# Performance work log

Hardware: AMD Instinct MI355X
Metric: run time of the kernel (lower is better)

Reference implementation:

```python
import jax, jax.numpy as jnp
import numpy as np

NUM_EXPERTS = 8
TOP_K = 2
HIDDEN = 2048
INTER = 2048
SWIGLU_LIMIT = 7.0
BATCH, SEQ = 4, 2048


def setup_inputs() -> dict:
    key = jax.random.key(0)
    k0, k1, k2, k3, k4 = jax.random.split(key, 5)
    x = jax.random.normal(k0, (BATCH, SEQ, HIDDEN), jnp.float32)
    Wr = jax.random.normal(k1, (HIDDEN, NUM_EXPERTS), jnp.float32) * 0.02
    Wg = jax.random.normal(k2, (NUM_EXPERTS, HIDDEN, INTER), jnp.float32) * 0.02
    Wu = jax.random.normal(k3, (NUM_EXPERTS, HIDDEN, INTER), jnp.float32) * 0.02
    Wd = jax.random.normal(k4, (NUM_EXPERTS, INTER, HIDDEN), jnp.float32) * 0.02
    return {"hidden_states": x, "Wr": Wr, "Wg": Wg, "Wu": Wu, "Wd": Wd}


def reference(hidden_states, Wr, Wg, Wu, Wd):
    # Router: logits [B,S,E], top-k over experts, softmax over the k logits.
    router_logits = jnp.einsum('bsh,he->bse', hidden_states, Wr)
    topk_logits, selected = jax.lax.top_k(router_logits, TOP_K)  # [B,S,K]
    router_probs = jax.nn.softmax(topk_logits, axis=-1)          # [B,S,K]

    # Per-expert masked-dense SwiGLU. Because the Dense layers have no bias,
    # Expert(x * mask) == Expert(x) at selected positions and the combine
    # weight is 0 elsewhere, so running on unmasked x is mathematically
    # identical to the original's masked-input formulation.
    out = jnp.zeros_like(hidden_states)
    for e in range(NUM_EXPERTS):  # fixed structural loop over experts
        w_e = jnp.where(selected == e, router_probs, 0.0).sum(axis=-1, keepdims=True)  # [B,S,1]
        g = jnp.einsum('bsh,hi->bsi', hidden_states, Wg[e])
        g = jnp.clip(jax.nn.silu(g), -SWIGLU_LIMIT, SWIGLU_LIMIT)
        u = jnp.einsum('bsh,hi->bsi', hidden_states, Wu[e])
        h = jnp.einsum('bsi,ih->bsh', g * u, Wd[e])
        out = out + h * w_e
    return out
```

## Files before the change

### kernel.cpp

```cpp
#include <hip/hip_runtime.h>

#define TOKENS 8192
#define HID 2048
#define NEXP 8
#define NT 32
#define MAXTILES 72

typedef float f32x4 __attribute__((ext_vector_type(4)));
typedef short bf16x8 __attribute__((ext_vector_type(8)));

#define WS_XBF     0ULL
#define WS_ACT     33554432ULL
#define WS_WCAT    100663296ULL
#define WS_WDT     234881024ULL
#define WS_ROWTOK  301989888ULL
#define WS_ROWPROB 302055424ULL
#define WS_EIDX    302120960ULL
#define WS_PROBS   302186496ULL
#define WS_META    302252032ULL
#define WS_SLOT    302253056ULL

__device__ __forceinline__ unsigned short f2bf(float f) {
    union { float f; unsigned int u; } a; a.f = f;
    unsigned int r = a.u + 0x7fffu + ((a.u >> 16) & 1u);
    return (unsigned short)(r >> 16);
}

__device__ __forceinline__ float bf2f(unsigned int lo16) {
    union { unsigned int u; float f; } x; x.u = lo16 << 16; return x.f;
}

__device__ __forceinline__ void gload16(void* ldsdst, const void* gsrc) {
    __builtin_amdgcn_global_load_lds(
        (const __attribute__((address_space(1))) void*)gsrc,
        (__attribute__((address_space(3))) void*)ldsdst, 16, 0, 0);
}

#define BAR asm volatile("s_barrier" ::: "memory")
#define VM4 asm volatile("s_waitcnt vmcnt(4)" ::: "memory")
#define VM0 asm volatile("s_waitcnt vmcnt(0)" ::: "memory")

__global__ __launch_bounds__(256) void router_kernel(
    const float* __restrict__ x, const float* __restrict__ Wr,
    unsigned short* __restrict__ xbf, int2* __restrict__ eidx,
    float2* __restrict__ probs, int* __restrict__ meta) {
    __shared__ float wrt[NEXP * HID];
    int tid = threadIdx.x;
    for (int f = tid; f < HID * NEXP; f += 256) {
        int i = f >> 3, e = f & 7;
        wrt[e * HID + i] = Wr[f];
    }
    __syncthreads();
    int w = tid >> 6, l = tid & 63;
#pragma unroll 1
    for (int ti = 0; ti < 4; ++ti) {
        int tok = blockIdx.x * 16 + w * 4 + ti;
        const float4* xr = (const float4*)(x + (size_t)tok * HID);
        float acc[NEXP];
#pragma unroll
        for (int e = 0; e < NEXP; ++e) acc[e] = 0.f;
        unsigned long long* xbr = (unsigned long long*)(xbf + (size_t)tok * HID);
#pragma unroll
        for (int it = 0; it < 8; ++it) {
            float4 v = xr[it * 64 + l];
            int k0 = (it * 64 + l) * 4;
#pragma unroll
            for (int e = 0; e < NEXP; ++e) {
                float4 wv = *(const float4*)&wrt[e * HID + k0];
                acc[e] += v.x * wv.x + v.y * wv.y + v.z * wv.z + v.w * wv.w;
            }
            unsigned long long pk = (unsigned long long)f2bf(v.x)
                                  | ((unsigned long long)f2bf(v.y) << 16)
                                  | ((unsigned long long)f2bf(v.z) << 32)
                                  | ((unsigned long long)f2bf(v.w) << 48);
            int qi = ((k0 >> 5) << 3) + (((k0 >> 2) & 3) << 1) + ((k0 >> 4) & 1);
            xbr[qi] = pk;
        }
#pragma unroll
        for (int e = 0; e < NEXP; ++e) {
#pragma unroll
            for (int d = 1; d < 64; d <<= 1) acc[e] += __shfl_xor(acc[e], d, 64);
        }
        if (l == 0) {
            int e0 = 0; float v0 = acc[0];
#pragma unroll
            for (int e = 1; e < NEXP; ++e) if (acc[e] > v0) { v0 = acc[e]; e0 = e; }
            int e1 = -1; float v1 = 0.f;
#pragma unroll
            for (int e = 0; e < NEXP; ++e)
                if (e != e0 && (e1 < 0 || acc[e] > v1)) { v1 = acc[e]; e1 = e; }
            float a = __expf(v1 - v0);
            float inv = 1.f / (1.f + a);
            int2 ei; ei.x = e0; ei.y = e1;
            float2 pp; pp.x = inv; pp.y = a * inv;
            eidx[tok] = ei;
            probs[tok] = pp;
            atomicAdd(&meta[e0], 1);
            atomicAdd(&meta[e1], 1);
        }
    }
}

__global__ __launch_bounds__(256) void convert_kernel(
    const float* __restrict__ Wg, const float* __restrict__ Wu,
    const float* __restrict__ Wd, unsigned short* __restrict__ wcat,
    unsigned short* __restrict__ wdt) {
    int mz = blockIdx.z;
    int mat = mz >> 3, e = mz & 7;
    const float* W = (mat == 0 ? Wg : (mat == 1 ? Wu : Wd)) + (size_t)e * HID * HID;
    int kb = blockIdx.y * 64, nb = blockIdx.x * 64;
    __shared__ unsigned short t[64][68];
    int tid = threadIdx.x;
    int kr = tid >> 4;
    int nc = (tid & 15) * 4;
#pragma unroll
    for (int ki = 0; ki < 4; ++ki) {
        int k = kr + ki * 16;
        float4 v = *(const float4*)&W[(size_t)(kb + k) * HID + nb + nc];
        t[nc + 0][k] = f2bf(v.x);
        t[nc + 1][k] = f2bf(v.y);
        t[nc + 2][k] = f2bf(v.z);
        t[nc + 3][k] = f2bf(v.w);
    }
    __syncthreads();
    int n = tid >> 2;
    int seg = tid & 3;
    int gn = nb + n;
    unsigned short* orow;
    if (mat < 2)
        orow = wcat + ((size_t)e * 4096 + (gn >> 4) * 32 + mat * 16 + (gn & 15)) * HID;
    else
        orow = wdt + ((size_t)e * HID + gn) * HID;
    unsigned long long pk[4];
#pragma unroll
    for (int j = 0; j < 4; ++j) {
        int qi = seg * 4 + j;
        int klocal = ((qi >> 3) << 5) + (((qi >> 1) & 3) << 2) + ((qi & 1) << 4);
        pk[j] = *(const unsigned long long*)&t[n][klocal];
    }
    unsigned long long* dst = (unsigned long long*)&orow[kb + seg * 16];
    dst[0] = pk[0]; dst[1] = pk[1]; dst[2] = pk[2]; dst[3] = pk[3];
}

__global__ void scan_kernel(int* __restrict__ meta) {
    if (threadIdx.x == 0) {
        int s = 0, tiles = 0;
#pragma unroll
        for (int e = 0; e < NEXP; ++e) {
            meta[16 + e] = s;
            int c = meta[e];
            int nt = (c + 255) >> 8;
            for (int i = 0; i < nt && tiles < MAXTILES; ++i)
                meta[32 + tiles++] = (e << 8) | i;
            s += c;
        }
        meta[24] = tiles;
    }
}

__global__ __launch_bounds__(256) void build_kernel(
    const int2* __restrict__ eidx, const float2* __restrict__ probs,
    int* __restrict__ meta, int* __restrict__ row_token, float* __restrict__ row_prob,
    int2* __restrict__ slots) {
    __shared__ int lc[NEXP], lbase[NEXP];
    int tid = threadIdx.x;
    if (tid < NEXP) lc[tid] = 0;
    __syncthreads();
    int t = blockIdx.x * 256 + tid;
    int2 e = eidx[t];
    float2 p = probs[t];
    int o0 = atomicAdd(&lc[e.x], 1);
    int o1 = atomicAdd(&lc[e.y], 1);
    __syncthreads();
    if (tid < NEXP) lbase[tid] = atomicAdd(&meta[8 + tid], lc[tid]);
    __syncthreads();
    int s0 = meta[16 + e.x] + lbase[e.x] + o0;
    int s1 = meta[16 + e.y] + lbase[e.y] + o1;
    row_token[s0] = t; row_prob[s0] = p.x;
    row_token[s1] = t; row_prob[s1] = p.y;
    int2 sl; sl.x = s0; sl.y = s1;
    slots[t] = sl;
}

#define STA(dn, kh, tt) { char* _d = lds + (dn)*32768 + (kh)*16384 + tid*16; \
    gload16(_d,        a0 + (tt)*64 + (kh)*32); \
    gload16(_d + 8192, a1 + (tt)*64 + (kh)*32); }
#define STB(dn, kh, tt) { char* _d = lds + (dn)*32768 + 65536 + (kh)*16384 + tid*16; \
    gload16(_d,        b0 + (tt)*64 + (kh)*32); \
    gload16(_d + 8192, b1 + (tt)*64 + (kh)*32); }
#define LDA_TO(dst, d, kh) { const char* _b = lds + (d)*32768 + (kh)*16384 + afo; \
    dst[0] = *(const bf16x8*)(_b);        dst[1] = *(const bf16x8*)(_b + 1024); \
    dst[2] = *(const bf16x8*)(_b + 2048); dst[3] = *(const bf16x8*)(_b + 3072); \
    dst[4] = *(const bf16x8*)(_b + 4096); dst[5] = *(const bf16x8*)(_b + 5120); \
    dst[6] = *(const bf16x8*)(_b + 6144); dst[7] = *(const bf16x8*)(_b + 7168); }
#define LDB(d, kh, nn) (*(const bf16x8*)(lds + (d)*32768 + (kh)*16384 + bfo + (nn)*1024))
#define MM(A, B0, B1, n0, n1) do { \
    __builtin_amdgcn_s_setprio(1); \
    _Pragma("unroll") \
    for (int m = 0; m < 8; ++m) { \
        acc[m][n0] = __builtin_amdgcn_mfma_f32_16x16x32_bf16(A[m], B0, acc[m][n0], 0, 0, 0); \
        acc[m][n1] = __builtin_amdgcn_mfma_f32_16x16x32_bf16(A[m], B1, acc[m][n1], 0, 0, 0); \
    } \
    __builtin_amdgcn_s_setprio(0); \
} while (0)

#define GEMM_MAIN_LOOP \
    f32x4 acc[8][4]; \
    { f32x4 z = {0.f,0.f,0.f,0.f}; \
      _Pragma("unroll") for (int m=0;m<8;++m) \
      _Pragma("unroll") for (int n=0;n<4;++n) acc[m][n]=z; } \
    bf16x8 af[8], af2[8], bq0, bq1, bq2, bq3; \
    STA(0, 0, 0); STB(0, 0, 0); STA(0, 1, 0); STB(0, 1, 0); \
    VM4; BAR; \
    LDA_TO(af, 0, 0); bq0 = LDB(0, 0, 0); bq1 = LDB(0, 0, 1); \
    for (int t = 0; t < NT - 1; ++t) { \
        const int d = t & 1, dn = d ^ 1, tn = t + 1; \
        bq2 = LDB(d, 0, 2); bq3 = LDB(d, 0, 3); \
        STA(dn, 0, tn); \
        MM(af, bq0, bq1, 0, 1); \
        STB(dn, 0, tn); \
        VM4; BAR; \
        LDA_TO(af2, d, 1); bq0 = LDB(d, 1, 0); bq1 = LDB(d, 1, 1); \
        MM(af, bq2, bq3, 2, 3); \
        bq2 = LDB(d, 1, 2); bq3 = LDB(d, 1, 3); \
        STA(dn, 1, tn); \
        MM(af2, bq0, bq1, 0, 1); \
        STB(dn, 1, tn); \
        VM4; BAR; \
        LDA_TO(af, dn, 0); bq0 = LDB(dn, 0, 0); bq1 = LDB(dn, 0, 1); \
        MM(af2, bq2, bq3, 2, 3); \
    } \
    { const int d = (NT - 1) & 1; \
        bq2 = LDB(d, 0, 2); bq3 = LDB(d, 0, 3); \
        MM(af, bq0, bq1, 0, 1); \
        VM0; BAR; \
        LDA_TO(af2, d, 1); bq0 = LDB(d, 1, 0); bq1 = LDB(d, 1, 1); \
        MM(af, bq2, bq3, 2, 3); \
        bq2 = LDB(d, 1, 2); bq3 = LDB(d, 1, 3); \
        MM(af2, bq0, bq1, 0, 1); \
        MM(af2, bq2, bq3, 2, 3); \
    }

__global__ __launch_bounds__(512, 2) void gemm1_kernel(
    const unsigned short* __restrict__ xbf, const unsigned short* __restrict__ wcat,
    const int* __restrict__ row_token, const int* __restrict__ meta,
    unsigned short* __restrict__ act) {
    int id = blockIdx.x;
    int sw = (id & 7) * 144 + (id >> 3);
    int ty = sw % MAXTILES;
    int ct = sw / MAXTILES;
    if (ty >= meta[24]) return;
    int mp = meta[32 + ty];
    int e = mp >> 8, rt = mp & 255;
    int cnt = meta[e];
    int off = meta[16 + e];
    __shared__ __align__(16) char lds[131072];
    int tid = threadIdx.x, w = tid >> 6, l = tid & 63;
    int wr = w >> 2, wc = w & 3;
    int r16 = l & 15, g = l >> 4;

    int srow = tid >> 2;
    int sxu = (tid & 3) ^ ((tid >> 3) & 3);
    int rr0 = rt * 256 + srow;       if (rr0 >= cnt) rr0 = cnt - 1;
    int rr1 = rt * 256 + srow + 128; if (rr1 >= cnt) rr1 = cnt - 1;
    const unsigned short* a0 = xbf + (size_t)row_token[off + rr0] * HID + sxu * 8;
    const unsigned short* a1 = xbf + (size_t)row_token[off + rr1] * HID + sxu * 8;
    const unsigned short* b0 = wcat + ((size_t)(e * 4096 + ct * 256 + srow)) * HID + sxu * 8;
    const unsigned short* b1 = b0 + (size_t)128 * HID;

    int swz = (r16 >> 1) & 3;
    int afo = (wr * 128 + r16) * 64 + (g ^ swz) * 16;
    int bfo = 65536 + (wc * 64 + r16) * 64 + (g ^ swz) * 16;

    GEMM_MAIN_LOOP

    int pb = (ct * 4 + wc) * 32 + (r16 >> 2) * 8 + (r16 & 3);
#pragma unroll
    for (int m = 0; m < 8; ++m) {
        int rbase = wr * 128 + m * 16 + (l >> 4) * 4;
#pragma unroll
        for (int q = 0; q < 4; ++q) {
            int r = rt * 256 + rbase + q;
            if (r < cnt) {
                unsigned short* arow = act + (size_t)(off + r) * HID;
#pragma unroll
                for (int p = 0; p < 2; ++p) {
                    float gg = acc[m][2 * p][q];
                    float uu = acc[m][2 * p + 1][q];
                    float s = gg / (1.f + __expf(-gg));
                    s = fminf(fmaxf(s, -7.f), 7.f);
                    arow[pb + p * 4] = f2bf(s * uu);
                }
            }
        }
    }
}

__global__ __launch_bounds__(512, 2) void gemm2_kernel(
    const unsigned short* __restrict__ act, const unsigned short* __restrict__ wdt,
    const int* __restrict__ meta, unsigned short* __restrict__ part) {
    int id = blockIdx.x;
    int sw = (id & 7) * 72 + (id >> 3);
    int ty = sw % MAXTILES;
    int ct = sw / MAXTILES;
    if (ty >= meta[24]) return;
    int mp = meta[32 + ty];
    int e = mp >> 8, rt = mp & 255;
    int cnt = meta[e];
    int off = meta[16 + e];
    __shared__ __align__(16) char lds[131072];
    int tid = threadIdx.x, w = tid >> 6, l = tid & 63;
    int wr = w >> 2, wc = w & 3;
    int r16 = l & 15, g = l >> 4;

    int srow = tid >> 2;
    int sxu = (tid & 3) ^ ((tid >> 3) & 3);
    int rr0 = rt * 256 + srow;       if (rr0 >= cnt) rr0 = cnt - 1;
    int rr1 = rt * 256 + srow + 128; if (rr1 >= cnt) rr1 = cnt - 1;
    const unsigned short* a0 = act + (size_t)(off + rr0) * HID + sxu * 8;
    const unsigned short* a1 = act + (size_t)(off + rr1) * HID + sxu * 8;
    const unsigned short* b0 = wdt + ((size_t)(e * HID + ct * 256 + srow)) * HID + sxu * 8;
    const unsigned short* b1 = b0 + (size_t)128 * HID;

    int swz = (r16 >> 1) & 3;
    int afo = (wr * 128 + r16) * 64 + (g ^ swz) * 16;
    int bfo = 65536 + (wc * 64 + r16) * 64 + (g ^ swz) * 16;

    GEMM_MAIN_LOOP

    int colb = ct * 256 + wc * 64;
#pragma unroll
    for (int m = 0; m < 8; ++m) {
        int rbase = wr * 128 + m * 16 + (l >> 4) * 4;
#pragma unroll
        for (int q = 0; q < 4; ++q) {
            int r = rt * 256 + rbase + q;
            if (r < cnt) {
                unsigned short* prow = part + (size_t)(off + r) * HID + colb;
#pragma unroll
                for (int nn = 0; nn < 4; ++nn)
                    prow[nn * 16 + r16] = f2bf(acc[m][nn][q]);
            }
        }
    }
}

__global__ __launch_bounds__(256) void combine_kernel(
    const unsigned short* __restrict__ part, const int2* __restrict__ slots,
    const float2* __restrict__ probs, float* __restrict__ out) {
    int t = blockIdx.x;
    int2 s = slots[t];
    float2 p = probs[t];
    int c = threadIdx.x * 8;
    uint4 a = *(const uint4*)(part + (size_t)s.x * HID + c);
    uint4 b = *(const uint4*)(part + (size_t)s.y * HID + c);
    unsigned au[4] = {a.x, a.y, a.z, a.w};
    unsigned bu[4] = {b.x, b.y, b.z, b.w};
    float res[8];
#pragma unroll
    for (int j = 0; j < 4; ++j) {
        res[2 * j]     = p.x * bf2f(au[j] & 0xffffu) + p.y * bf2f(bu[j] & 0xffffu);
        res[2 * j + 1] = p.x * bf2f(au[j] >> 16)     + p.y * bf2f(bu[j] >> 16);
    }
    float* o = out + (size_t)t * HID + c;
    float4 o0 = {res[0], res[1], res[2], res[3]};
    float4 o1 = {res[4], res[5], res[6], res[7]};
    *(float4*)o = o0;
    *(float4*)(o + 4) = o1;
}

extern "C" void kernel_launch(void* const* d_in, const int* in_sizes, int n_in,
                              void* d_out, int out_size, void* d_ws, size_t ws_size,
                              hipStream_t stream) {
    const float* x  = (const float*)d_in[0];
    const float* Wr = (const float*)d_in[1];
    const float* Wg = (const float*)d_in[2];
    const float* Wu = (const float*)d_in[3];
    const float* Wd = (const float*)d_in[4];
    float* out = (float*)d_out;
    char* ws = (char*)d_ws;

    unsigned short* xbf  = (unsigned short*)(ws + WS_XBF);
    unsigned short* act  = (unsigned short*)(ws + WS_ACT);
    unsigned short* wcat = (unsigned short*)(ws + WS_WCAT);
    unsigned short* part = (unsigned short*)(ws + WS_WCAT);
    unsigned short* wdt  = (unsigned short*)(ws + WS_WDT);
    int* row_token  = (int*)(ws + WS_ROWTOK);
    float* row_prob = (float*)(ws + WS_ROWPROB);
    int2* eidx      = (int2*)(ws + WS_EIDX);
    float2* probs   = (float2*)(ws + WS_PROBS);
    int* meta       = (int*)(ws + WS_META);
    int2* slots     = (int2*)(ws + WS_SLOT);

    hipMemsetAsync(meta, 0, 64, stream);

    hipLaunchKernelGGL(convert_kernel, dim3(32, 32, 24), dim3(256), 0, stream,
                       Wg, Wu, Wd, wcat, wdt);
    hipLaunchKernelGGL(router_kernel, dim3(TOKENS / 16), dim3(256), 0, stream,
                       x, Wr, xbf, eidx, probs, meta);
    hipLaunchKernelGGL(scan_kernel, dim3(1), dim3(64), 0, stream, meta);
    hipLaunchKernelGGL(build_kernel, dim3(TOKENS / 256), dim3(256), 0, stream,
                       eidx, probs, meta, row_token, row_prob, slots);
    hipLaunchKernelGGL(gemm1_kernel, dim3(16 * MAXTILES), dim3(512), 0, stream,
                       xbf, wcat, row_token, meta, act);
    hipLaunchKernelGGL(gemm2_kernel, dim3(8 * MAXTILES), dim3(512), 0, stream,
                       act, wdt, meta, part);
    hipLaunchKernelGGL(combine_kernel, dim3(TOKENS), dim3(256), 0, stream,
                       part, slots, probs, out);
}
```

Measured before the change: 779.2 us.

## Fuse router and weight conversion into one prep kernel with larger tiles

Merges the router/x-to-bf16 kernel and the weight conversion/transpose kernel into a single launch, with the first 512 blocks doing routing and the rest converting weights. Conversion tiles grow from 64x64 to 128x128, so each block moves more data and there are fewer blocks. The intent is to remove one launch boundary, let routing overlap with the bandwidth-bound weight conversion, and cut per-block overhead. In exchange the 64KB shared allocation applies to every block, which may lower occupancy for the conversion blocks. The slot workspace offset is also shifted.

```diff
diff --git a/kernel.cpp b/kernel.cpp
--- a/kernel.cpp
+++ b/kernel.cpp
@@ -18,7 +18,7 @@
 #define WS_EIDX    302120960ULL
 #define WS_PROBS   302186496ULL
 #define WS_META    302252032ULL
-#define WS_SLOT    302253056ULL
+#define WS_SLOT    302253568ULL
 
 __device__ __forceinline__ unsigned short f2bf(float f) {
     union { float f; unsigned int u; } a; a.f = f;
@@ -40,106 +40,111 @@
 #define VM4 asm volatile("s_waitcnt vmcnt(4)" ::: "memory")
 #define VM0 asm volatile("s_waitcnt vmcnt(0)" ::: "memory")
 
-__global__ __launch_bounds__(256) void router_kernel(
+__global__ __launch_bounds__(256) void prep_kernel(
     const float* __restrict__ x, const float* __restrict__ Wr,
-    unsigned short* __restrict__ xbf, int2* __restrict__ eidx,
-    float2* __restrict__ probs, int* __restrict__ meta) {
-    __shared__ float wrt[NEXP * HID];
+    const float* __restrict__ Wg, const float* __restrict__ Wu,
+    const float* __restrict__ Wd, unsigned short* __restrict__ xbf,
+    int2* __restrict__ eidx, float2* __restrict__ probs,
+    int* __restrict__ meta, unsigned short* __restrict__ wcat,
+    unsigned short* __restrict__ wdt) {
+    __shared__ __align__(16) char smem[65536];
     int tid = threadIdx.x;
-    for (int f = tid; f < HID * NEXP; f += 256) {
-        int i = f >> 3, e = f & 7;
-        wrt[e * HID + i] = Wr[f];
-    }
-    __syncthreads();
-    int w = tid >> 6, l = tid & 63;
+    int id = blockIdx.x;
+
+    if (id < 512) {
+        float* wrt = (float*)smem;
+        for (int f = tid; f < HID * NEXP; f += 256) {
+            int i = f >> 3, e = f & 7;
+            wrt[e * HID + i] = Wr[f];
+        }
+        __syncthreads();
+        int w = tid >> 6, l = tid & 63;
 #pragma unroll 1
-    for (int ti = 0; ti < 4; ++ti) {
-        int tok = blockIdx.x * 16 + w * 4 + ti;
-        const float4* xr = (const float4*)(x + (size_t)tok * HID);
-        float acc[NEXP];
-#pragma unroll
-        for (int e = 0; e < NEXP; ++e) acc[e] = 0.f;
-        unsigned long long* xbr = (unsigned long long*)(xbf + (size_t)tok * HID);
-#pragma unroll
-        for (int it = 0; it < 8; ++it) {
-            float4 v = xr[it * 64 + l];
-            int k0 = (it * 64 + l) * 4;
+        for (int ti = 0; ti < 4; ++ti) {
+            int tok = id * 16 + w * 4 + ti;
+            const float4* xr = (const float4*)(x + (size_t)tok * HID);
+            float acc[NEXP];
+#pragma unroll
+            for (int e = 0; e < NEXP; ++e) acc[e] = 0.f;
+            unsigned long long* xbr = (unsigned long long*)(xbf + (size_t)tok * HID);
+#pragma unroll
+            for (int it = 0; it < 8; ++it) {
+                float4 v = xr[it * 64 + l];
+                int k0 = (it * 64 + l) * 4;
+#pragma unroll
+                for (int e = 0; e < NEXP; ++e) {
+                    float4 wv = *(const float4*)&wrt[e * HID + k0];
+                    acc[e] += v.x * wv.x + v.y * wv.y + v.z * wv.z + v.w * wv.w;
+                }
+                unsigned long long pk = (unsigned long long)f2bf(v.x)
+                                      | ((unsigned long long)f2bf(v.y) << 16)
+                                      | ((unsigned long long)f2bf(v.z) << 32)
+                                      | ((unsigned long long)f2bf(v.w) << 48);
+                int qi = ((k0 >> 5) << 3) + (((k0 >> 2) & 3) << 1) + ((k0 >> 4) & 1);
+                xbr[qi] = pk;
+            }
 #pragma unroll
             for (int e = 0; e < NEXP; ++e) {
-                float4 wv = *(const float4*)&wrt[e * HID + k0];
-                acc[e] += v.x * wv.x + v.y * wv.y + v.z * wv.z + v.w * wv.w;
+#pragma unroll
+                for (int d = 1; d < 64; d <<= 1) acc[e] += __shfl_xor(acc[e], d, 64);
             }
-            unsigned long long pk = (unsigned long long)f2bf(v.x)
-                                  | ((unsigned long long)f2bf(v.y) << 16)
-                                  | ((unsigned long long)f2bf(v.z) << 32)
-                                  | ((unsigned long long)f2bf(v.w) << 48);
-            int qi = ((k0 >> 5) << 3) + (((k0 >> 2) & 3) << 1) + ((k0 >> 4) & 1);
-            xbr[qi] = pk;
-        }
-#pragma unroll
-        for (int e = 0; e < NEXP; ++e) {
-#pragma unroll
-            for (int d = 1; d < 64; d <<= 1) acc[e] += __shfl_xor(acc[e], d, 64);
-        }
-        if (l == 0) {
-            int e0 = 0; float v0 = acc[0];
-#pragma unroll
-            for (int e = 1; e < NEXP; ++e) if (acc[e] > v0) { v0 = acc[e]; e0 = e; }
-            int e1 = -1; float v1 = 0.f;
-#pragma unroll
-            for (int e = 0; e < NEXP; ++e)
-                if (e != e0 && (e1 < 0 || acc[e] > v1)) { v1 = acc[e]; e1 = e; }
-            float a = __expf(v1 - v0);
-            float inv = 1.f / (1.f + a);
-            int2 ei; ei.x = e0; ei.y = e1;
-            float2 pp; pp.x = inv; pp.y = a * inv;
-            eidx[tok] = ei;
-            probs[tok] = pp;
-            atomicAdd(&meta[e0], 1);
-            atomicAdd(&meta[e1], 1);
-        }
-    }
-}
-
-__global__ __launch_bounds__(256) void convert_kernel(
-    const float* __restrict__ Wg, const float* __restrict__ Wu,
-    const float* __restrict__ Wd, unsigned short* __restrict__ wcat,
-    unsigned short* __restrict__ wdt) {
-    int mz = blockIdx.z;
-    int mat = mz >> 3, e = mz & 7;
-    const float* W = (mat == 0 ? Wg : (mat == 1 ? Wu : Wd)) + (size_t)e * HID * HID;
-    int kb = blockIdx.y * 64, nb = blockIdx.x * 64;
-    __shared__ unsigned short t[64][68];
-    int tid = threadIdx.x;
-    int kr = tid >> 4;
-    int nc = (tid & 15) * 4;
-#pragma unroll
-    for (int ki = 0; ki < 4; ++ki) {
-        int k = kr + ki * 16;
-        float4 v = *(const float4*)&W[(size_t)(kb + k) * HID + nb + nc];
-        t[nc + 0][k] = f2bf(v.x);
-        t[nc + 1][k] = f2bf(v.y);
-        t[nc + 2][k] = f2bf(v.z);
-        t[nc + 3][k] = f2bf(v.w);
-    }
-    __syncthreads();
-    int n = tid >> 2;
-    int seg = tid & 3;
-    int gn = nb + n;
-    unsigned short* orow;
-    if (mat < 2)
-        orow = wcat + ((size_t)e * 4096 + (gn >> 4) * 32 + mat * 16 + (gn & 15)) * HID;
-    else
-        orow = wdt + ((size_t)e * HID + gn) * HID;
-    unsigned long long pk[4];
-#pragma unroll
-    for (int j = 0; j < 4; ++j) {
-        int qi = seg * 4 + j;
-        int klocal = ((qi >> 3) << 5) + (((qi >> 1) & 3) << 2) + ((qi & 1) << 4);
-        pk[j] = *(const unsigned long long*)&t[n][klocal];
-    }
-    unsigned long long* dst = (unsigned long long*)&orow[kb + seg * 16];
-    dst[0] = pk[0]; dst[1] = pk[1]; dst[2] = pk[2]; dst[3] = pk[3];
+            if (l == 0) {
+                int e0 = 0; float v0 = acc[0];
+#pragma unroll
+                for (int e = 1; e < NEXP; ++e) if (acc[e] > v0) { v0 = acc[e]; e0 = e; }
+                int e1 = -1; float v1 = 0.f;
+#pragma unroll
+                for (int e = 0; e < NEXP; ++e)
+                    if (e != e0 && (e1 < 0 || acc[e] > v1)) { v1 = acc[e]; e1 = e; }
+                float a = __expf(v1 - v0);
+                float inv = 1.f / (1.f + a);
+                int2 ei; ei.x = e0; ei.y = e1;
+                float2 pp; pp.x = inv; pp.y = a * inv;
+                eidx[tok] = ei;
+                probs[tok] = pp;
+                atomicAdd(&meta[e0], 1);
+                atomicAdd(&meta[e1], 1);
+            }
+        }
+    } else {
+        int cid = id - 512;
+        int nb = (cid & 15) * 128;
+        int kb = ((cid >> 4) & 15) * 128;
+        int mz = cid >> 8;
+        int mat = mz >> 3, e = mz & 7;
+        const float* W = (mat == 0 ? Wg : (mat == 1 ? Wu : Wd)) + (size_t)e * HID * HID;
+        unsigned short (*t)[132] = (unsigned short (*)[132])smem;
+        int nc = (tid & 31) * 4;
+        int kr = tid >> 5;
+#pragma unroll
+        for (int ki = 0; ki < 16; ++ki) {
+            int k = kr + ki * 8;
+            float4 v = *(const float4*)&W[(size_t)(kb + k) * HID + nb + nc];
+            t[nc + 0][k] = f2bf(v.x);
+            t[nc + 1][k] = f2bf(v.y);
+            t[nc + 2][k] = f2bf(v.z);
+            t[nc + 3][k] = f2bf(v.w);
+        }
+        __syncthreads();
+        int n = tid >> 1;
+        int seg = tid & 1;
+        int gn = nb + n;
+        unsigned short* orow;
+        if (mat < 2)
+            orow = wcat + ((size_t)e * 4096 + (gn >> 4) * 32 + mat * 16 + (gn & 15)) * HID;
+        else
+            orow = wdt + ((size_t)e * HID + gn) * HID;
+        unsigned long long pk[16];
+#pragma unroll
+        for (int j = 0; j < 16; ++j) {
+            int qi = seg * 16 + j;
+            int klocal = ((qi >> 3) << 5) + (((qi >> 1) & 3) << 2) + ((qi & 1) << 4);
+            pk[j] = *(const unsigned long long*)&t[n][klocal];
+        }
+        unsigned long long* dst = (unsigned long long*)&orow[kb + seg * 64];
+#pragma unroll
+        for (int j = 0; j < 16; ++j) dst[j] = pk[j];
+    }
 }
 
 __global__ void scan_kernel(int* __restrict__ meta) {
@@ -394,10 +399,8 @@
 
     hipMemsetAsync(meta, 0, 64, stream);
 
-    hipLaunchKernelGGL(convert_kernel, dim3(32, 32, 24), dim3(256), 0, stream,
-                       Wg, Wu, Wd, wcat, wdt);
-    hipLaunchKernelGGL(router_kernel, dim3(TOKENS / 16), dim3(256), 0, stream,
-                       x, Wr, xbf, eidx, probs, meta);
+    hipLaunchKernelGGL(prep_kernel, dim3(512 + 6144), dim3(256), 0, stream,
+                       x, Wr, Wg, Wu, Wd, xbf, eidx, probs, meta, wcat, wdt);
     hipLaunchKernelGGL(scan_kernel, dim3(1), dim3(64), 0, stream, meta);
     hipLaunchKernelGGL(build_kernel, dim3(TOKENS / 256), dim3(256), 0, stream,
                        eidx, probs, meta, row_token, row_prob, slots);
```

After: 788.2 us. Within noise of the previous version (+1.1%).
